# Optimization experiments

Measured on AMD Instinct MI355X. Metric: run time of the kernel, lower is better.

## Reference

```python
import jax, jax.numpy as jnp
import numpy as np

B, N, MAX_DEG = 256, 512, 6
F_IN, H = 62, 128  # layers = [62, 128, 128]
NUM_DEG = MAX_DEG + 1  # degree buckets 0..6


def gather_neighbors(atoms, edges, maskvalue):
    # atoms [B,N,F], edges [B,N,D] with -1 padding -> [B,N,D,F]
    idx = jnp.maximum(edges, 0)
    neigh = jax.vmap(lambda a, e: a[e])(atoms, idx)
    return jnp.where(edges[..., None] < 0, jnp.asarray(maskvalue, atoms.dtype), neigh)


def nfp_conv(atoms, edges, W, b):
    # W [NUM_DEG, F_in, F_out], b [NUM_DEG, F_out]
    deg = jnp.sum(edges >= 0, axis=-1)  # [B,N]
    neigh = gather_neighbors(atoms, edges, 0.0)
    summed = neigh.sum(axis=2) + atoms  # include self, [B,N,F_in]
    out = jnp.zeros(summed.shape[:2] + (W.shape[-1],), summed.dtype)
    for d in range(NUM_DEG):  # small fixed set of degree buckets
        h = jax.nn.sigmoid(summed @ W[d] + b[d])
        out = out + h * (deg == d)[..., None].astype(h.dtype)
    return out


def graph_pool(atoms, edges):
    # max over self + neighbors
    neigh = gather_neighbors(atoms, edges, -jnp.inf)
    allf = jnp.concatenate([atoms[:, :, None, :], neigh], axis=2)  # [B,N,D+1,F]
    return allf.max(axis=2)


def setup_inputs() -> dict:
    key = jax.random.key(0)
    ka, ke, km, k0, k1, k2, k3 = jax.random.split(key, 7)
    a = jax.random.normal(ka, (B, N, F_IN), dtype=jnp.float32)
    e = jax.random.randint(ke, (B, N, MAX_DEG), 0, N, dtype=jnp.int32)
    # introduce -1 padding so atoms have varied degrees 0..6
    u = jax.random.uniform(km, (B, N, MAX_DEG))
    e = jnp.where(u < 0.6, e, -1).astype(jnp.int32)
    W0 = jax.random.normal(k0, (NUM_DEG, F_IN, H), dtype=jnp.float32) * 0.1
    b0 = jax.random.normal(k1, (NUM_DEG, H), dtype=jnp.float32) * 0.1
    W1 = jax.random.normal(k2, (NUM_DEG, H, H), dtype=jnp.float32) * 0.1
    b1 = jax.random.normal(k3, (NUM_DEG, H), dtype=jnp.float32) * 0.1
    return {"a": a, "e": e, "W0": W0, "b0": b0, "W1": W1, "b1": b1}


def reference(a, e, W0, b0, W1, b1):
    x = nfp_conv(a, e, W0, b0)
    x = graph_pool(x, e)
    x = nfp_conv(x, e, W1, b1)
    x = graph_pool(x, e)
    return x.sum(axis=1)  # SubgraphSum: [B, H]
```

## Files before the change

kernel.cpp:

```cpp
#include <hip/hip_runtime.h>
#include <math.h>

#define BB 256
#define NN 512
#define DD 6
#define F_IN 62
#define HH 128
#define ND 7
#define TOTAL (BB*NN)
#define OPB 640
#define OPBS 624
#define GPB 40
#define TPB 10

typedef __bf16 bf16x8 __attribute__((ext_vector_type(8)));
typedef float f32x4 __attribute__((ext_vector_type(4)));

__device__ __forceinline__ unsigned short f2bf(float f) {
    unsigned u = __builtin_bit_cast(unsigned, f);
    u = (u + 0x7FFFu + ((u >> 16) & 1u)) >> 16;
    return (unsigned short)u;
}
__device__ __forceinline__ float lo2f(unsigned x) { return __builtin_bit_cast(float, x << 16); }
__device__ __forceinline__ float hi2f(unsigned x) { return __builtin_bit_cast(float, x & 0xFFFF0000u); }

__device__ __forceinline__ uint4 pack8(const float* s) {
    uint4 r;
    r.x = (unsigned)f2bf(s[0]) | ((unsigned)f2bf(s[1]) << 16);
    r.y = (unsigned)f2bf(s[2]) | ((unsigned)f2bf(s[3]) << 16);
    r.z = (unsigned)f2bf(s[4]) | ((unsigned)f2bf(s[5]) << 16);
    r.w = (unsigned)f2bf(s[6]) | ((unsigned)f2bf(s[7]) << 16);
    return r;
}
__device__ __forceinline__ void unpack_add(float* s, uint4 q) {
    s[0] += lo2f(q.x); s[1] += hi2f(q.x); s[2] += lo2f(q.y); s[3] += hi2f(q.y);
    s[4] += lo2f(q.z); s[5] += hi2f(q.z); s[6] += lo2f(q.w); s[7] += hi2f(q.w);
}
__device__ __forceinline__ void unpack_max(float* s, uint4 q) {
    s[0] = fmaxf(s[0], lo2f(q.x)); s[1] = fmaxf(s[1], hi2f(q.x));
    s[2] = fmaxf(s[2], lo2f(q.y)); s[3] = fmaxf(s[3], hi2f(q.y));
    s[4] = fmaxf(s[4], lo2f(q.z)); s[5] = fmaxf(s[5], hi2f(q.z));
    s[6] = fmaxf(s[6], lo2f(q.w)); s[7] = fmaxf(s[7], hi2f(q.w));
}


__global__ __launch_bounds__(512) void k_sort16(const int* __restrict__ e,
                                                int* __restrict__ order,
                                                int* __restrict__ inv,
                                                int* __restrict__ dgrp,
                                                int* __restrict__ ntiles) {
    __shared__ unsigned int scnt[ND];
    __shared__ unsigned int sbase[ND + 1];
    const int b = blockIdx.x;
    const int t = threadIdx.x;
    if (t < ND) scnt[t] = 0u;
    for (int i = t; i < OPB; i += 512) order[b * OPB + i] = -1;
    __syncthreads();
    int d = 0;
#pragma unroll
    for (int j = 0; j < DD; ++j) d += (e[(b * NN + t) * DD + j] >= 0) ? 1 : 0;
    unsigned rk = atomicAdd(&scnt[d], 1u);
    __syncthreads();
    if (t == 0) {
        unsigned acc = 0;
        for (int k = 0; k < ND; ++k) { sbase[k] = acc; acc += (scnt[k] + 15u) & ~15u; }
        sbase[ND] = acc;
        for (int k = 0; k < ND; ++k)
            for (unsigned g = sbase[k] >> 4; g < (sbase[k + 1] >> 4); ++g)
                dgrp[b * GPB + g] = k;
        for (unsigned g = sbase[ND] >> 4; g < GPB; ++g) dgrp[b * GPB + g] = 0;
        ntiles[b] = (int)((sbase[ND] + 63u) >> 6);
    }
    __syncthreads();
    const int slot = (int)(sbase[d] + rk);
    order[b * OPB + slot] = t;
    inv[b * NN + t] = slot;
}


__global__ void k_prep_wt(const float* __restrict__ W, unsigned short* __restrict__ WT,
                          int F, int K) {
    int n = blockIdx.x;
    int d = blockIdx.y;
    for (int k = threadIdx.x; k < K; k += 64) {
        float v = (k < F) ? W[((size_t)d * F + k) * HH + n] : 0.f;
        WT[((size_t)d * HH + n) * K + k] = f2bf(v);
    }
}


__global__ __launch_bounds__(512)
void k_gather1(const float* __restrict__ a, const int* __restrict__ e,
               const int* __restrict__ order, const int* __restrict__ ntiles,
               unsigned short* __restrict__ S1) {
    const int t = threadIdx.x;
    const int bi = blockIdx.x;
    const int x8 = bi & 7;
    const int j = bi >> 3;
    const int batch = x8 + 8 * (j / TPB);
    const int blk = j % TPB;
    if (blk >= ntiles[batch]) return;
    const int slot = blk * 64 + (t >> 3);
    const int kb = t & 7;
    const int v = order[batch * OPB + slot];
    if (v < 0) return;
    const int* ep = e + ((size_t)batch * NN + v) * DD;
    const float* base = a + (size_t)batch * NN * F_IN;
    float s[8] = {0.f, 0.f, 0.f, 0.f, 0.f, 0.f, 0.f, 0.f};
    {
        const float* r = base + (size_t)v * F_IN + kb * 8;
        float2 z0 = *(const float2*)(r);     s[0] += z0.x; s[1] += z0.y;
        float2 z1 = *(const float2*)(r + 2); s[2] += z1.x; s[3] += z1.y;
        float2 z2 = *(const float2*)(r + 4); s[4] += z2.x; s[5] += z2.y;
        if (kb < 7) { float2 z3 = *(const float2*)(r + 6); s[6] += z3.x; s[7] += z3.y; }
    }
#pragma unroll
    for (int jj = 0; jj < DD; ++jj) {
        int idx = ep[jj];
        if (idx >= 0) {
            const float* r = base + (size_t)idx * F_IN + kb * 8;
            float2 z0 = *(const float2*)(r);     s[0] += z0.x; s[1] += z0.y;
            float2 z1 = *(const float2*)(r + 2); s[2] += z1.x; s[3] += z1.y;
            float2 z2 = *(const float2*)(r + 4); s[4] += z2.x; s[5] += z2.y;
            if (kb < 7) { float2 z3 = *(const float2*)(r + 6); s[6] += z3.x; s[7] += z3.y; }
        }
    }
    *(uint4*)(S1 + ((size_t)batch * OPBS + slot) * 64 + kb * 8) = pack8(s);
}


__global__ __launch_bounds__(512)
void k_gather2(const unsigned short* __restrict__ P1, const int* __restrict__ e,
               const int* __restrict__ order, const int* __restrict__ ntiles,
               unsigned short* __restrict__ S2) {
    constexpr int BPB2 = 20;
    const int t = threadIdx.x;
    const int bi = blockIdx.x;
    const int x8 = bi & 7;
    const int j = bi >> 3;
    const int batch = x8 + 8 * (j / BPB2);
    const int blk = j % BPB2;
    if ((blk >> 1) >= ntiles[batch]) return;
    const int slot = blk * 32 + (t >> 4);
    const int kb = t & 15;
    const int v = order[batch * OPB + slot];
    if (v < 0) return;
    const int* ep = e + ((size_t)batch * NN + v) * DD;
    const unsigned short* base = P1 + (size_t)batch * NN * HH + kb * 8;
    float s[8] = {0.f, 0.f, 0.f, 0.f, 0.f, 0.f, 0.f, 0.f};
    unpack_add(s, *(const uint4*)(base + (size_t)v * HH));
#pragma unroll
    for (int jj = 0; jj < DD; ++jj) {
        int idx = ep[jj];
        if (idx >= 0) unpack_add(s, *(const uint4*)(base + (size_t)idx * HH));
    }
    *(uint4*)(S2 + ((size_t)batch * OPBS + slot) * HH + kb * 8) = pack8(s);
}


template<int KB>
__global__ __launch_bounds__(512, 4)
void k_gemm(const unsigned short* __restrict__ S,
            const unsigned short* __restrict__ WT, const float* __restrict__ bias,
            const int* __restrict__ dgrp, const int* __restrict__ ntiles,
            unsigned short* __restrict__ Y) {
    constexpr int K = KB * 8;
    constexpr int LOGKB = (KB == 16) ? 4 : 3;
    __shared__ unsigned short sP[64 * 128];

    const int t = threadIdx.x;
    const int l = t & 63;
    const int w = t >> 6;

    const int bi = blockIdx.x;
    const int x8 = bi & 7;
    const int j = bi >> 3;
    const int batch = x8 + 8 * (j / TPB);
    const int tile = j % TPB;
    if (tile >= ntiles[batch]) return;

    for (int u = t; u < 64 * KB; u += 512) {
        const int n = u >> LOGKB;
        const int kb = u & (KB - 1);
        int slot = tile * 64 + n;
        if (slot >= OPBS) slot = OPBS - 1;
        const unsigned short* src = S + ((size_t)batch * OPBS + slot) * K + kb * 8;
        *(uint4*)&sP[(n * KB + (kb ^ (n & 7))) * 8] = *(const uint4*)src;
    }
    __syncthreads();

    const int lr = l & 15;
    const int lq = l >> 4;
    const int mb = w >> 1;
    const int col0 = (w & 1) * 64;
    const int d = dgrp[batch * GPB + tile * 4 + mb];
    const int nrow = mb * 16 + lr;

    bf16x8 af[K / 32];
#pragma unroll
    for (int kk = 0; kk < K / 32; ++kk)
        af[kk] = *(const bf16x8*)&sP[(nrow * KB + ((kk * 4 + lq) ^ (nrow & 7))) * 8];

    f32x4 acc[4];
#pragma unroll
    for (int fr = 0; fr < 4; ++fr) { f32x4 z = {0.f, 0.f, 0.f, 0.f}; acc[fr] = z; }
#pragma unroll
    for (int fr = 0; fr < 4; ++fr) {
        const unsigned short* wp = WT + ((size_t)d * HH + col0 + fr * 16 + lr) * K + lq * 8;
#pragma unroll
        for (int kk = 0; kk < K / 32; ++kk) {
            bf16x8 bfr = *(const bf16x8*)(wp + kk * 32);
            acc[fr] = __builtin_amdgcn_mfma_f32_16x16x32_bf16(af[kk], bfr, acc[fr], 0, 0, 0);
        }
    }

    __syncthreads();
#pragma unroll
    for (int fr = 0; fr < 4; ++fr) {
        const int col = col0 + fr * 16 + lr;
        const float bv = bias[d * HH + col];
#pragma unroll
        for (int r = 0; r < 4; ++r) {
            const int n = mb * 16 + lq * 4 + r;
            float z = 1.f / (1.f + __expf(-(acc[fr][r] + bv)));
            sP[n * HH + col] = f2bf(z);
        }
    }
    __syncthreads();
    for (int u = t; u < 1024; u += 512) {
        const int n = u >> 4;
        const int c8 = (u & 15) * 8;
        const int slot = tile * 64 + n;
        if (slot < OPBS) {
            uint4 p = *(const uint4*)&sP[n * HH + c8];
            *(uint4*)&Y[((size_t)batch * OPBS + slot) * HH + c8] = p;
        }
    }
}


__global__ __launch_bounds__(256) void k_pool_bf(const unsigned short* __restrict__ Xs,
                                                 const int* __restrict__ e,
                                                 const int* __restrict__ inv,
                                                 unsigned short* __restrict__ P) {
    const int t = threadIdx.x;
    const int bi = blockIdx.x;
    const int x8 = bi & 7;
    const int j = bi >> 3;
    const int batch = x8 + 8 * (j >> 5);
    const int sub = j & 31;
    const int node = sub * 16 + (t >> 4);
    const int u = batch * NN + node;
    const int c8 = (t & 15) * 8;
    const unsigned short* base = Xs + (size_t)batch * OPBS * HH + c8;
    float m[8];
    {
        uint4 p = *(const uint4*)(base + (size_t)inv[u] * HH);
        m[0] = lo2f(p.x); m[1] = hi2f(p.x); m[2] = lo2f(p.y); m[3] = hi2f(p.y);
        m[4] = lo2f(p.z); m[5] = hi2f(p.z); m[6] = lo2f(p.w); m[7] = hi2f(p.w);
    }
#pragma unroll
    for (int jj = 0; jj < DD; ++jj) {
        int idx = e[u * DD + jj];
        if (idx >= 0) unpack_max(m, *(const uint4*)(base + (size_t)inv[batch * NN + idx] * HH));
    }
    *(uint4*)&P[(size_t)u * HH + c8] = pack8(m);
}


__global__ __launch_bounds__(256) void k_pool_sum_part(const unsigned short* __restrict__ Xs,
                                                       const int* __restrict__ e,
                                                       const int* __restrict__ inv,
                                                       float* __restrict__ partial) {
    __shared__ float red[16][HH + 4];
    const int t = threadIdx.x;
    const int bi = blockIdx.x;
    const int x8 = bi & 7;
    const int j = bi >> 3;
    const int b = x8 + 8 * (j >> 5);
    const int chunk = j & 31;
    const int slot = t >> 4;
    const int c8 = (t & 15) * 8;

    const int u = b * NN + chunk * 16 + slot;
    const unsigned short* base = Xs + (size_t)b * OPBS * HH + c8;
    float m[8];
    {
        uint4 p = *(const uint4*)(base + (size_t)inv[u] * HH);
        m[0] = lo2f(p.x); m[1] = hi2f(p.x); m[2] = lo2f(p.y); m[3] = hi2f(p.y);
        m[4] = lo2f(p.z); m[5] = hi2f(p.z); m[6] = lo2f(p.w); m[7] = hi2f(p.w);
    }
#pragma unroll
    for (int jj = 0; jj < DD; ++jj) {
        int idx = e[u * DD + jj];
        if (idx >= 0) unpack_max(m, *(const uint4*)(base + (size_t)inv[b * NN + idx] * HH));
    }
#pragma unroll
    for (int i = 0; i < 8; ++i) red[slot][c8 + i] = m[i];
    __syncthreads();
    if (t < HH) {
        float s = 0.f;
#pragma unroll
        for (int k = 0; k < 16; ++k) s += red[k][t];
        partial[((size_t)b * 32 + chunk) * HH + t] = s;
    }
}


__global__ __launch_bounds__(256) void k_sum_final(const float* __restrict__ partial,
                                                   float* __restrict__ out) {
    int g = blockIdx.x * 256 + threadIdx.x;
    int b = g >> 7;
    int c = g & 127;
    float s = 0.f;
#pragma unroll
    for (int k = 0; k < 32; ++k) s += partial[((size_t)b * 32 + k) * HH + c];
    out[g] = s;
}


extern "C" void kernel_launch(void* const* d_in, const int* in_sizes, int n_in,
                              void* d_out, int out_size, void* d_ws, size_t ws_size,
                              hipStream_t stream) {
    const float* a  = (const float*)d_in[0];
    const int*   e  = (const int*)d_in[1];
    const float* W0 = (const float*)d_in[2];
    const float* b0 = (const float*)d_in[3];
    const float* W1 = (const float*)d_in[4];
    const float* b1 = (const float*)d_in[5];
    float* out = (float*)d_out;

    char* ws = (char*)d_ws;
    const size_t SB = (size_t)BB * OPBS * HH * 2;
    unsigned short* bufA = (unsigned short*)ws;
    unsigned short* bufB = (unsigned short*)(ws + SB);
    float* partial = (float*)bufA;
    char* dp = ws + 2 * SB;
    unsigned short* WT0 = (unsigned short*)dp;
    unsigned short* WT1 = WT0 + (size_t)ND * HH * 64;
    int* order  = (int*)(WT1 + (size_t)ND * HH * 128);
    int* dgrp   = order + (size_t)BB * OPB;
    int* ntiles = dgrp + (size_t)BB * GPB;
    int* inv    = ntiles + 256;

    hipLaunchKernelGGL(k_sort16, dim3(BB), dim3(NN), 0, stream, e, order, inv, dgrp, ntiles);
    hipLaunchKernelGGL(k_prep_wt, dim3(HH, ND), dim3(64), 0, stream, W0, WT0, F_IN, 64);
    hipLaunchKernelGGL(k_prep_wt, dim3(HH, ND), dim3(64), 0, stream, W1, WT1, HH, HH);

    hipLaunchKernelGGL(k_gather1, dim3(BB * TPB), dim3(512), 0, stream,
                       a, e, order, ntiles, bufB);
    hipLaunchKernelGGL((k_gemm<8>), dim3(BB * TPB), dim3(512), 0, stream,
                       bufB, WT0, b0, dgrp, ntiles, bufA);
    hipLaunchKernelGGL(k_pool_bf, dim3(TOTAL / 16), dim3(256), 0, stream, bufA, e, inv, bufB);
    hipLaunchKernelGGL(k_gather2, dim3(BB * 20), dim3(512), 0, stream,
                       bufB, e, order, ntiles, bufA);
    hipLaunchKernelGGL((k_gemm<16>), dim3(BB * TPB), dim3(512), 0, stream,
                       bufA, WT1, b1, dgrp, ntiles, bufB);
    hipLaunchKernelGGL(k_pool_sum_part, dim3(BB * 32), dim3(256), 0, stream, bufB, e, inv, partial);
    hipLaunchKernelGGL(k_sum_final, dim3(BB * HH / 256), dim3(256), 0, stream, partial, out);
}
```

Baseline: 181.0 us.

## Fuse neighbor gather into the degree-bucketed MFMA GEMM kernel

Merges the separate gather kernels into the GEMM kernels. Each wave now gathers and sums its 16 rows' neighbor features directly into MFMA A-fragments in registers, then multiplies by the degree-specific weights and writes the sigmoid output through shared staging. This removes the bf16 intermediate buffer round trip through global memory and two kernel launches. In exchange it drops the early exit on empty tiles (always 5 blocks of 128 rows per batch), pads the slot stride to 640, and has each wave compute all 128 output columns with weights loaded straight from global memory.

Measured after the change: 184.7 us. 2.0% more time.

```diff
diff --git a/kernel.cpp b/kernel.cpp
--- a/kernel.cpp
+++ b/kernel.cpp
@@ -9,9 +9,9 @@
 #define ND 7
 #define TOTAL (BB*NN)
 #define OPB 640
-#define OPBS 624
+#define SSTR 640
 #define GPB 40
-#define TPB 10
+#define STG 132
 
 typedef __bf16 bf16x8 __attribute__((ext_vector_type(8)));
 typedef float f32x4 __attribute__((ext_vector_type(4)));
@@ -42,13 +42,18 @@
     s[4] = fmaxf(s[4], lo2f(q.z)); s[5] = fmaxf(s[5], hi2f(q.z));
     s[6] = fmaxf(s[6], lo2f(q.w)); s[7] = fmaxf(s[7], hi2f(q.w));
 }
+__device__ __forceinline__ void rowadd62(float* s, const float* r, int kb) {
+    float2 z0 = *(const float2*)(r);     s[0] += z0.x; s[1] += z0.y;
+    float2 z1 = *(const float2*)(r + 2); s[2] += z1.x; s[3] += z1.y;
+    float2 z2 = *(const float2*)(r + 4); s[4] += z2.x; s[5] += z2.y;
+    if (kb < 7) { float2 z3 = *(const float2*)(r + 6); s[6] += z3.x; s[7] += z3.y; }
+}
 
 
 __global__ __launch_bounds__(512) void k_sort16(const int* __restrict__ e,
                                                 int* __restrict__ order,
                                                 int* __restrict__ inv,
-                                                int* __restrict__ dgrp,
-                                                int* __restrict__ ntiles) {
+                                                int* __restrict__ dgrp) {
     __shared__ unsigned int scnt[ND];
     __shared__ unsigned int sbase[ND + 1];
     const int b = blockIdx.x;
@@ -69,7 +74,6 @@
             for (unsigned g = sbase[k] >> 4; g < (sbase[k + 1] >> 4); ++g)
                 dgrp[b * GPB + g] = k;
         for (unsigned g = sbase[ND] >> 4; g < GPB; ++g) dgrp[b * GPB + g] = 0;
-        ntiles[b] = (int)((sbase[ND] + 63u) >> 6);
     }
     __syncthreads();
     const int slot = (int)(sbase[d] + rk);
@@ -89,152 +93,89 @@
 }
 
 
-__global__ __launch_bounds__(512)
-void k_gather1(const float* __restrict__ a, const int* __restrict__ e,
-               const int* __restrict__ order, const int* __restrict__ ntiles,
-               unsigned short* __restrict__ S1) {
-    const int t = threadIdx.x;
+template<int KB>
+__global__ __launch_bounds__(512, 4)
+void k_conv_nb(const void* __restrict__ Xin, const int* __restrict__ e,
+               const unsigned short* __restrict__ WT, const float* __restrict__ bias,
+               const int* __restrict__ order, const int* __restrict__ dgrp,
+               unsigned short* __restrict__ Ys) {
+    constexpr int K = KB * 8;
+    constexpr int KK = KB / 4;
+    __shared__ unsigned short stg[128 * STG];
+
+    const int t = threadIdx.x;
+    const int l = t & 63;
+    const int w = t >> 6;
+    const int lr = l & 15;
+    const int lq = l >> 4;
+
     const int bi = blockIdx.x;
     const int x8 = bi & 7;
     const int j = bi >> 3;
-    const int batch = x8 + 8 * (j / TPB);
-    const int blk = j % TPB;
-    if (blk >= ntiles[batch]) return;
-    const int slot = blk * 64 + (t >> 3);
-    const int kb = t & 7;
+    const int batch = x8 + 8 * (j / 5);
+    const int blk = j % 5;
+    const int g = blk * 8 + w;
+    const int slot = g * 16 + lr;
+
     const int v = order[batch * OPB + slot];
-    if (v < 0) return;
-    const int* ep = e + ((size_t)batch * NN + v) * DD;
-    const float* base = a + (size_t)batch * NN * F_IN;
-    float s[8] = {0.f, 0.f, 0.f, 0.f, 0.f, 0.f, 0.f, 0.f};
+    const int d = dgrp[batch * GPB + g];
+
+    int eidx[DD];
     {
-        const float* r = base + (size_t)v * F_IN + kb * 8;
-        float2 z0 = *(const float2*)(r);     s[0] += z0.x; s[1] += z0.y;
-        float2 z1 = *(const float2*)(r + 2); s[2] += z1.x; s[3] += z1.y;
-        float2 z2 = *(const float2*)(r + 4); s[4] += z2.x; s[5] += z2.y;
-        if (kb < 7) { float2 z3 = *(const float2*)(r + 6); s[6] += z3.x; s[7] += z3.y; }
-    }
-#pragma unroll
-    for (int jj = 0; jj < DD; ++jj) {
-        int idx = ep[jj];
-        if (idx >= 0) {
-            const float* r = base + (size_t)idx * F_IN + kb * 8;
-            float2 z0 = *(const float2*)(r);     s[0] += z0.x; s[1] += z0.y;
-            float2 z1 = *(const float2*)(r + 2); s[2] += z1.x; s[3] += z1.y;
-            float2 z2 = *(const float2*)(r + 4); s[4] += z2.x; s[5] += z2.y;
-            if (kb < 7) { float2 z3 = *(const float2*)(r + 6); s[6] += z3.x; s[7] += z3.y; }
+        const int* ep = e + ((size_t)batch * NN + (v >= 0 ? v : 0)) * DD;
+#pragma unroll
+        for (int jj = 0; jj < DD; ++jj) eidx[jj] = (v >= 0) ? ep[jj] : -1;
+    }
+
+    bf16x8 af[KK];
+#pragma unroll
+    for (int kk = 0; kk < KK; ++kk) {
+        const int kb = lq + 4 * kk;
+        float s[8] = {0.f, 0.f, 0.f, 0.f, 0.f, 0.f, 0.f, 0.f};
+        if (v >= 0) {
+            if constexpr (KB == 16) {
+                const unsigned short* base = (const unsigned short*)Xin
+                                             + (size_t)batch * NN * HH + kb * 8;
+                unpack_add(s, *(const uint4*)(base + (size_t)v * HH));
+#pragma unroll
+                for (int jj = 0; jj < DD; ++jj)
+                    if (eidx[jj] >= 0)
+                        unpack_add(s, *(const uint4*)(base + (size_t)eidx[jj] * HH));
+            } else {
+                const float* base = (const float*)Xin + (size_t)batch * NN * F_IN + kb * 8;
+                rowadd62(s, base + (size_t)v * F_IN, kb);
+#pragma unroll
+                for (int jj = 0; jj < DD; ++jj)
+                    if (eidx[jj] >= 0) rowadd62(s, base + (size_t)eidx[jj] * F_IN, kb);
+            }
         }
-    }
-    *(uint4*)(S1 + ((size_t)batch * OPBS + slot) * 64 + kb * 8) = pack8(s);
-}
-
-
-__global__ __launch_bounds__(512)
-void k_gather2(const unsigned short* __restrict__ P1, const int* __restrict__ e,
-               const int* __restrict__ order, const int* __restrict__ ntiles,
-               unsigned short* __restrict__ S2) {
-    constexpr int BPB2 = 20;
-    const int t = threadIdx.x;
-    const int bi = blockIdx.x;
-    const int x8 = bi & 7;
-    const int j = bi >> 3;
-    const int batch = x8 + 8 * (j / BPB2);
-    const int blk = j % BPB2;
-    if ((blk >> 1) >= ntiles[batch]) return;
-    const int slot = blk * 32 + (t >> 4);
-    const int kb = t & 15;
-    const int v = order[batch * OPB + slot];
-    if (v < 0) return;
-    const int* ep = e + ((size_t)batch * NN + v) * DD;
-    const unsigned short* base = P1 + (size_t)batch * NN * HH + kb * 8;
-    float s[8] = {0.f, 0.f, 0.f, 0.f, 0.f, 0.f, 0.f, 0.f};
-    unpack_add(s, *(const uint4*)(base + (size_t)v * HH));
-#pragma unroll
-    for (int jj = 0; jj < DD; ++jj) {
-        int idx = ep[jj];
-        if (idx >= 0) unpack_add(s, *(const uint4*)(base + (size_t)idx * HH));
-    }
-    *(uint4*)(S2 + ((size_t)batch * OPBS + slot) * HH + kb * 8) = pack8(s);
-}
-
-
-template<int KB>
-__global__ __launch_bounds__(512, 4)
-void k_gemm(const unsigned short* __restrict__ S,
-            const unsigned short* __restrict__ WT, const float* __restrict__ bias,
-            const int* __restrict__ dgrp, const int* __restrict__ ntiles,
-            unsigned short* __restrict__ Y) {
-    constexpr int K = KB * 8;
-    constexpr int LOGKB = (KB == 16) ? 4 : 3;
-    __shared__ unsigned short sP[64 * 128];
-
-    const int t = threadIdx.x;
-    const int l = t & 63;
-    const int w = t >> 6;
-
-    const int bi = blockIdx.x;
-    const int x8 = bi & 7;
-    const int j = bi >> 3;
-    const int batch = x8 + 8 * (j / TPB);
-    const int tile = j % TPB;
-    if (tile >= ntiles[batch]) return;
-
-    for (int u = t; u < 64 * KB; u += 512) {
-        const int n = u >> LOGKB;
-        const int kb = u & (KB - 1);
-        int slot = tile * 64 + n;
-        if (slot >= OPBS) slot = OPBS - 1;
-        const unsigned short* src = S + ((size_t)batch * OPBS + slot) * K + kb * 8;
-        *(uint4*)&sP[(n * KB + (kb ^ (n & 7))) * 8] = *(const uint4*)src;
-    }
-    __syncthreads();
-
-    const int lr = l & 15;
-    const int lq = l >> 4;
-    const int mb = w >> 1;
-    const int col0 = (w & 1) * 64;
-    const int d = dgrp[batch * GPB + tile * 4 + mb];
-    const int nrow = mb * 16 + lr;
-
-    bf16x8 af[K / 32];
-#pragma unroll
-    for (int kk = 0; kk < K / 32; ++kk)
-        af[kk] = *(const bf16x8*)&sP[(nrow * KB + ((kk * 4 + lq) ^ (nrow & 7))) * 8];
-
-    f32x4 acc[4];
-#pragma unroll
-    for (int fr = 0; fr < 4; ++fr) { f32x4 z = {0.f, 0.f, 0.f, 0.f}; acc[fr] = z; }
-#pragma unroll
-    for (int fr = 0; fr < 4; ++fr) {
-        const unsigned short* wp = WT + ((size_t)d * HH + col0 + fr * 16 + lr) * K + lq * 8;
-#pragma unroll
-        for (int kk = 0; kk < K / 32; ++kk) {
+        uint4 r = pack8(s);
+        af[kk] = __builtin_bit_cast(bf16x8, r);
+    }
+
+#pragma unroll
+    for (int fr = 0; fr < 8; ++fr) {
+        const unsigned short* wp = WT + ((size_t)d * HH + fr * 16 + lr) * K + lq * 8;
+        f32x4 z = {0.f, 0.f, 0.f, 0.f};
+#pragma unroll
+        for (int kk = 0; kk < KK; ++kk) {
             bf16x8 bfr = *(const bf16x8*)(wp + kk * 32);
-            acc[fr] = __builtin_amdgcn_mfma_f32_16x16x32_bf16(af[kk], bfr, acc[fr], 0, 0, 0);
+            z = __builtin_amdgcn_mfma_f32_16x16x32_bf16(af[kk], bfr, z, 0, 0, 0);
         }
-    }
-
-    __syncthreads();
-#pragma unroll
-    for (int fr = 0; fr < 4; ++fr) {
-        const int col = col0 + fr * 16 + lr;
-        const float bv = bias[d * HH + col];
-#pragma unroll
-        for (int r = 0; r < 4; ++r) {
-            const int n = mb * 16 + lq * 4 + r;
-            float z = 1.f / (1.f + __expf(-(acc[fr][r] + bv)));
-            sP[n * HH + col] = f2bf(z);
+        const float bv = bias[d * HH + fr * 16 + lr];
+#pragma unroll
+        for (int r2 = 0; r2 < 4; ++r2) {
+            float zz = 1.f / (1.f + __expf(-(z[r2] + bv)));
+            stg[(w * 16 + lq * 4 + r2) * STG + fr * 16 + lr] = f2bf(zz);
         }
     }
-    __syncthreads();
-    for (int u = t; u < 1024; u += 512) {
+
+    __syncthreads();
+    for (int u = t; u < 2048; u += 512) {
         const int n = u >> 4;
         const int c8 = (u & 15) * 8;
-        const int slot = tile * 64 + n;
-        if (slot < OPBS) {
-            uint4 p = *(const uint4*)&sP[n * HH + c8];
-            *(uint4*)&Y[((size_t)batch * OPBS + slot) * HH + c8] = p;
-        }
+        uint4 p = *(const uint4*)&stg[n * STG + c8];
+        *(uint4*)&Ys[((size_t)batch * SSTR + blk * 128 + n) * HH + c8] = p;
     }
 }
 
@@ -252,7 +193,7 @@
     const int node = sub * 16 + (t >> 4);
     const int u = batch * NN + node;
     const int c8 = (t & 15) * 8;
-    const unsigned short* base = Xs + (size_t)batch * OPBS * HH + c8;
+    const unsigned short* base = Xs + (size_t)batch * SSTR * HH + c8;
     float m[8];
     {
         uint4 p = *(const uint4*)(base + (size_t)inv[u] * HH);
@@ -283,7 +224,7 @@
     const int c8 = (t & 15) * 8;
 
     const int u = b * NN + chunk * 16 + slot;
-    const unsigned short* base = Xs + (size_t)b * OPBS * HH + c8;
+    const unsigned short* base = Xs + (size_t)b * SSTR * HH + c8;
     float m[8];
     {
         uint4 p = *(const uint4*)(base + (size_t)inv[u] * HH);
@@ -331,31 +272,26 @@
     float* out = (float*)d_out;
 
     char* ws = (char*)d_ws;
-    const size_t SB = (size_t)BB * OPBS * HH * 2;
+    const size_t SA = (size_t)BB * SSTR * HH * 2;
     unsigned short* bufA = (unsigned short*)ws;
-    unsigned short* bufB = (unsigned short*)(ws + SB);
-    float* partial = (float*)bufA;
-    char* dp = ws + 2 * SB;
+    unsigned short* bufB = (unsigned short*)(ws + SA);
+    float* partial = (float*)bufB;
+    char* dp = ws + SA + (size_t)TOTAL * HH * 2;
     unsigned short* WT0 = (unsigned short*)dp;
     unsigned short* WT1 = WT0 + (size_t)ND * HH * 64;
-    int* order  = (int*)(WT1 + (size_t)ND * HH * 128);
-    int* dgrp   = order + (size_t)BB * OPB;
-    int* ntiles = dgrp + (size_t)BB * GPB;
-    int* inv    = ntiles + 256;
-
-    hipLaunchKernelGGL(k_sort16, dim3(BB), dim3(NN), 0, stream, e, order, inv, dgrp, ntiles);
+    int* order = (int*)(WT1 + (size_t)ND * HH * 128);
+    int* dgrp  = order + (size_t)BB * OPB;
+    int* inv   = dgrp + (size_t)BB * GPB;
+
+    hipLaunchKernelGGL(k_sort16, dim3(BB), dim3(NN), 0, stream, e, order, inv, dgrp);
     hipLaunchKernelGGL(k_prep_wt, dim3(HH, ND), dim3(64), 0, stream, W0, WT0, F_IN, 64);
     hipLaunchKernelGGL(k_prep_wt, dim3(HH, ND), dim3(64), 0, stream, W1, WT1, HH, HH);
 
-    hipLaunchKernelGGL(k_gather1, dim3(BB * TPB), dim3(512), 0, stream,
-                       a, e, order, ntiles, bufB);
-    hipLaunchKernelGGL((k_gemm<8>), dim3(BB * TPB), dim3(512), 0, stream,
-                       bufB, WT0, b0, dgrp, ntiles, bufA);
+    hipLaunchKernelGGL((k_conv_nb<8>),  dim3(BB * 5), dim3(512), 0, stream,
+                       (const void*)a, e, WT0, b0, order, dgrp, bufA);
     hipLaunchKernelGGL(k_pool_bf, dim3(TOTAL / 16), dim3(256), 0, stream, bufA, e, inv, bufB);
-    hipLaunchKernelGGL(k_gather2, dim3(BB * 20), dim3(512), 0, stream,
-                       bufB, e, order, ntiles, bufA);
-    hipLaunchKernelGGL((k_gemm<16>), dim3(BB * TPB), dim3(512), 0, stream,
-                       bufA, WT1, b1, dgrp, ntiles, bufB);
-    hipLaunchKernelGGL(k_pool_sum_part, dim3(BB * 32), dim3(256), 0, stream, bufB, e, inv, partial);
+    hipLaunchKernelGGL((k_conv_nb<16>), dim3(BB * 5), dim3(512), 0, stream,
+                       (const void*)bufB, e, WT1, b1, order, dgrp, bufA);
+    hipLaunchKernelGGL(k_pool_sum_part, dim3(BB * 32), dim3(256), 0, stream, bufA, e, inv, partial);
     hipLaunchKernelGGL(k_sum_final, dim3(BB * HH / 256), dim3(256), 0, stream, partial, out);
 }
```
